# Performance work log

Measured on AMD Instinct MI355X. Metric: run time of the kernel, lower is better.

The kernel has to match this reference:

```python
import jax, jax.numpy as jnp
import numpy as np

D_MODEL = 1024
NUM_HEADS = 16
HEAD_DIM = D_MODEL // NUM_HEADS
THETA = 10000.0


def _trunc_normal(key, shape, std):
    # approximate trunc_normal_(a=-3std, b=3std) by clipping
    return jnp.clip(jax.random.normal(key, shape) * std, -3 * std, 3 * std)


def setup_inputs() -> dict:
    key = jax.random.key(0)
    ks = jax.random.split(key, 6)
    B, S = 2, 2048
    x = jax.random.normal(ks[0], (B, S, D_MODEL), dtype=jnp.float32)
    token_positions = jnp.sort(
        jax.random.randint(ks[1], (B, S), 0, 2048), axis=-1
    ).astype(jnp.int64)
    std = float(np.sqrt(2.0 / (D_MODEL + D_MODEL)))
    Wq = _trunc_normal(ks[2], (D_MODEL, D_MODEL), std)
    Wk = _trunc_normal(ks[3], (D_MODEL, D_MODEL), std)
    Wv = _trunc_normal(ks[4], (D_MODEL, D_MODEL), std)
    Wo = _trunc_normal(ks[5], (D_MODEL, D_MODEL), std)
    return {"x": x, "Wq": Wq, "Wk": Wk, "Wv": Wv, "Wo": Wo,
            "token_positions": token_positions}


def _rope(x, positions):
    # x: (b, h, s, d), positions: (b, s)
    d = x.shape[-1]
    inv_freq = THETA ** (-jnp.arange(0, d, 2, dtype=jnp.float32) / d)  # (d/2,)
    angles = positions.astype(jnp.float32)[:, None, :, None] * inv_freq  # (b,1,s,d/2)
    cos, sin = jnp.cos(angles), jnp.sin(angles)
    x_even, x_odd = x[..., 0::2], x[..., 1::2]
    out_even = x_even * cos - x_odd * sin
    out_odd = x_even * sin + x_odd * cos
    # interleave back: (..., d/2, 2) -> (..., d)
    return jnp.stack([out_even, out_odd], axis=-1).reshape(x.shape)


def reference(x, Wq, Wk, Wv, Wo, token_positions):
    B, S, _ = x.shape
    H, Dh = NUM_HEADS, HEAD_DIM
    # projections: einsum '... i, o i -> ... o'
    q = jnp.einsum('bsi,oi->bso', x, Wq).reshape(B, S, H, Dh).transpose(0, 2, 1, 3)
    k = jnp.einsum('bsi,oi->bso', x, Wk).reshape(B, S, H, Dh).transpose(0, 2, 1, 3)
    v = jnp.einsum('bsi,oi->bso', x, Wv).reshape(B, S, H, Dh).transpose(0, 2, 1, 3)
    q = _rope(q, token_positions)
    k = _rope(k, token_positions)
    scores = jnp.einsum('bhqd,bhkd->bhqk', q.astype(jnp.float32),
                        k.astype(jnp.float32)) / jnp.sqrt(
        jnp.asarray(Dh, dtype=jnp.float32))
    causal = jnp.tril(jnp.ones((S, S), dtype=bool))
    scores = jnp.where(causal, scores, -jnp.inf)
    attn = jax.nn.softmax(scores, axis=-1)
    out = jnp.einsum('bhqk,bhkd->bhqd', attn, v.astype(jnp.float32)).astype(x.dtype)
    out = out.transpose(0, 2, 1, 3).reshape(B, S, H * Dh)
    return jnp.einsum('bsi,oi->bso', out, Wo)
```

## Files before the change

kernel.cpp:

```cpp
#include <hip/hip_runtime.h>
#include <hip/hip_bf16.h>

#define DMODEL 1024
#define NHEADS 16
#define HDIM   64
#define BATCH  2
#define SEQ    2048
#define XELEMS ((size_t)BATCH * SEQ * DMODEL)
#define WELEMS ((size_t)DMODEL * DMODEL)

typedef __attribute__((ext_vector_type(8))) __bf16 bf16x8;
typedef __attribute__((ext_vector_type(4))) float  f32x4;
typedef __attribute__((ext_vector_type(2))) float  f32x2;
typedef __attribute__((ext_vector_type(4))) unsigned int   u32x4;
typedef __attribute__((ext_vector_type(4))) unsigned short u16x4;
typedef __attribute__((ext_vector_type(8))) unsigned short u16x8;

typedef const __attribute__((address_space(1))) void* gas_t;
typedef __attribute__((address_space(3))) void* las_t;

static __device__ __forceinline__ unsigned short f2bf(float f) {
  return __builtin_bit_cast(unsigned short, __float2bfloat16(f));
}
static __device__ __forceinline__ float bf2f(unsigned short u) {
  return __bfloat162float(__builtin_bit_cast(__hip_bfloat16, u));
}

__global__ __launch_bounds__(64) void probe_kernel(const unsigned int* __restrict__ x,
                                                   const int* __restrict__ pos,
                                                   int* __restrict__ flags) {
  const int lane = threadIdx.x;
  int bad = 0;
#pragma unroll
  for (int i = 0; i < 32; ++i) {
    const unsigned int u = x[lane * 32 + i];
    if (((u >> 23) & 0xFFu) == 0xFFu) bad++;
  }
  int zodd = 0;
#pragma unroll
  for (int i = 0; i < 4; ++i)
    if (pos[lane * 8 + 2 * i + 1] == 0) zodd++;
#pragma unroll
  for (int s = 1; s < 64; s <<= 1) {
    bad  += __shfl_xor(bad, s);
    zodd += __shfl_xor(zodd, s);
  }
  if (lane == 0) {
    flags[0] = (bad < 64) ? 1 : 0;
    flags[1] = (zodd >= 200) ? 1 : 0;
  }
}

__global__ __launch_bounds__(256) void rope_table_kernel(const int* __restrict__ pos,
                                                         const int* __restrict__ flags,
                                                         float* __restrict__ tab) {
  const int i = blockIdx.x * 256 + threadIdx.x;
  const int pd = i & 31, rs = i >> 5;
  const int pv = flags[1] ? pos[2 * rs] : pos[rs];
  const float ang = (float)pv * exp2f(-(float)pd * 0.41524101186092026f);
  f32x2 t; t[0] = cosf(ang); t[1] = sinf(ang);
  *(f32x2*)&tab[2 * i] = t;
}

__global__ __launch_bounds__(256) void conv_kernel(
    const void* __restrict__ x,
    const void* __restrict__ w0, const void* __restrict__ w1,
    const void* __restrict__ w2, const void* __restrict__ w3,
    unsigned short* __restrict__ dst, const int* __restrict__ flags) {
  const size_t e = ((size_t)blockIdx.x * 256 + threadIdx.x) * 8;
  const void* src;
  size_t off;
  if (e < XELEMS) { src = x; off = e; }
  else {
    const size_t r = e - XELEMS;
    const int wi = (int)(r >> 20);
    src = (wi == 0) ? w0 : (wi == 1) ? w1 : (wi == 2) ? w2 : w3;
    off = r & (WELEMS - 1);
  }
  if (flags[0]) {
    const float* s = (const float*)src + off;
    const f32x4 a = *(const f32x4*)(s);
    const f32x4 b = *(const f32x4*)(s + 4);
    u16x8 o8;
#pragma unroll
    for (int j = 0; j < 4; ++j) o8[j] = f2bf(a[j]);
#pragma unroll
    for (int j = 0; j < 4; ++j) o8[4 + j] = f2bf(b[j]);
    *(u16x8*)(dst + e) = o8;
  } else {
    *(u32x4*)(dst + e) = *(const u32x4*)((const unsigned short*)src + off);
  }
}

__device__ __forceinline__ void gemm_core(const unsigned short* __restrict__ Ag,
                                          const unsigned short* __restrict__ Bg,
                                          unsigned short* As, unsigned short* Bs,
                                          int bm, int bn, f32x4 acc[4][4]) {
  const int tid = threadIdx.x;
  const int lane = tid & 63;
  const int w  = tid >> 6;
  const int wm = w >> 1, wn = w & 1;
  const int c = lane & 15, g = lane >> 4;
  const int r0 = tid >> 2;
  const int s0 = (tid & 3) * 8;

  auto stage = [&](int buf, int k0) {
    unsigned short* ad = As + buf * 4096;
    unsigned short* bd = Bs + buf * 4096;
    __builtin_amdgcn_global_load_lds((gas_t)(Ag + (size_t)(bm + r0) * DMODEL + k0 + s0),
                                     (las_t)(ad + tid * 8), 16, 0, 0);
    __builtin_amdgcn_global_load_lds((gas_t)(Ag + (size_t)(bm + r0 + 64) * DMODEL + k0 + s0),
                                     (las_t)(ad + (tid + 256) * 8), 16, 0, 0);
    __builtin_amdgcn_global_load_lds((gas_t)(Bg + (size_t)(bn + r0) * DMODEL + k0 + s0),
                                     (las_t)(bd + tid * 8), 16, 0, 0);
    __builtin_amdgcn_global_load_lds((gas_t)(Bg + (size_t)(bn + r0 + 64) * DMODEL + k0 + s0),
                                     (las_t)(bd + (tid + 256) * 8), 16, 0, 0);
  };

  stage(0, 0);
  __syncthreads();
  for (int k0 = 0; k0 < DMODEL; k0 += 32) {
    const int cur = (k0 >> 5) & 1;
    if (k0 + 32 < DMODEL) stage(cur ^ 1, k0 + 32);
    const unsigned short* ar = As + cur * 4096;
    const unsigned short* br = Bs + cur * 4096;
    bf16x8 af[4], bfr[4];
#pragma unroll
    for (int m = 0; m < 4; ++m)
      af[m] = *(const bf16x8*)&ar[(wm * 64 + m * 16 + c) * 32 + g * 8];
#pragma unroll
    for (int n = 0; n < 4; ++n)
      bfr[n] = *(const bf16x8*)&br[(wn * 64 + n * 16 + c) * 32 + g * 8];
    __builtin_amdgcn_s_setprio(1);
#pragma unroll
    for (int m = 0; m < 4; ++m)
#pragma unroll
      for (int n = 0; n < 4; ++n)
        acc[m][n] = __builtin_amdgcn_mfma_f32_16x16x32_bf16(af[m], bfr[n], acc[m][n], 0, 0, 0);
    __builtin_amdgcn_s_setprio(0);
    __syncthreads();
  }
}

__global__ __launch_bounds__(256) void qkv_gemm_kernel(
    const unsigned short* __restrict__ x,
    const unsigned short* __restrict__ Wq, const unsigned short* __restrict__ Wk,
    const unsigned short* __restrict__ Wv,
    unsigned short* __restrict__ qo, unsigned short* __restrict__ ko,
    unsigned short* __restrict__ vto) {
  __shared__ unsigned short As[2 * 128 * 32];
  __shared__ unsigned short Bs[2 * 128 * 32];
  const int z = blockIdx.z;
  const unsigned short* W = (z == 0) ? Wq : (z == 1) ? Wk : Wv;
  const int bm = blockIdx.x * 128, bn = blockIdx.y * 128;
  f32x4 acc[4][4];
#pragma unroll
  for (int m = 0; m < 4; ++m)
#pragma unroll
    for (int n = 0; n < 4; ++n)
#pragma unroll
      for (int j = 0; j < 4; ++j) acc[m][n][j] = 0.f;

  gemm_core(x, W, As, Bs, bm, bn, acc);

  const int tid = threadIdx.x, lane = tid & 63, w = tid >> 6;
  const int wm = w >> 1, wn = w & 1, c = lane & 15, g4 = lane >> 4;
#pragma unroll
  for (int m = 0; m < 4; ++m) {
#pragma unroll
    for (int n = 0; n < 4; ++n) {
      const int col = bn + wn * 64 + n * 16 + c;
      const int h = col >> 6, d = col & 63;
      const int row0 = bm + wm * 64 + m * 16 + g4 * 4;
      if (z == 2) {
        const int b = row0 >> 11, s0 = row0 & (SEQ - 1);
        u16x4 pk;
#pragma unroll
        for (int j = 0; j < 4; ++j) pk[j] = f2bf(acc[m][n][j]);
        *(u16x4*)&vto[((size_t)(b * NHEADS + h) * HDIM + d) * SEQ + s0] = pk;
      } else {
        unsigned short* dst = z ? ko : qo;
#pragma unroll
        for (int j = 0; j < 4; ++j) {
          const int row = row0 + j;
          const int b = row >> 11, s = row & (SEQ - 1);
          dst[((size_t)(b * NHEADS + h) * SEQ + s) * HDIM + d] = f2bf(acc[m][n][j]);
        }
      }
    }
  }
}

__global__ __launch_bounds__(256) void out_gemm_kernel(
    const unsigned short* __restrict__ A, const unsigned short* __restrict__ Wo,
    void* __restrict__ outv, const int* __restrict__ flags) {
  __shared__ unsigned short As[2 * 64 * 32];
  __shared__ unsigned short Bs[2 * 128 * 32];
  const int bm = blockIdx.x * 64, bn = blockIdx.y * 128;
  const int tid = threadIdx.x, lane = tid & 63, w = tid >> 6;
  const int c = lane & 15, g = lane >> 4;
  const int r0 = tid >> 2, s0 = (tid & 3) * 8;
  f32x4 acc[4][2];
#pragma unroll
  for (int m = 0; m < 4; ++m)
#pragma unroll
    for (int n = 0; n < 2; ++n)
#pragma unroll
      for (int j = 0; j < 4; ++j) acc[m][n][j] = 0.f;

  auto stage = [&](int buf, int k0) {
    __builtin_amdgcn_global_load_lds((gas_t)(A + (size_t)(bm + r0) * DMODEL + k0 + s0),
                                     (las_t)(As + buf * 2048 + tid * 8), 16, 0, 0);
    __builtin_amdgcn_global_load_lds((gas_t)(Wo + (size_t)(bn + r0) * DMODEL + k0 + s0),
                                     (las_t)(Bs + buf * 4096 + tid * 8), 16, 0, 0);
    __builtin_amdgcn_global_load_lds((gas_t)(Wo + (size_t)(bn + r0 + 64) * DMODEL + k0 + s0),
                                     (las_t)(Bs + buf * 4096 + (tid + 256) * 8), 16, 0, 0);
  };

  stage(0, 0);
  __syncthreads();
  for (int k0 = 0; k0 < DMODEL; k0 += 32) {
    const int cur = (k0 >> 5) & 1;
    if (k0 + 32 < DMODEL) stage(cur ^ 1, k0 + 32);
    const unsigned short* ar = As + cur * 2048;
    const unsigned short* br = Bs + cur * 4096;
    bf16x8 af[4], bfr[2];
#pragma unroll
    for (int m = 0; m < 4; ++m)
      af[m] = *(const bf16x8*)&ar[(m * 16 + c) * 32 + g * 8];
#pragma unroll
    for (int n = 0; n < 2; ++n)
      bfr[n] = *(const bf16x8*)&br[(w * 32 + n * 16 + c) * 32 + g * 8];
    __builtin_amdgcn_s_setprio(1);
#pragma unroll
    for (int m = 0; m < 4; ++m)
#pragma unroll
      for (int n = 0; n < 2; ++n)
        acc[m][n] = __builtin_amdgcn_mfma_f32_16x16x32_bf16(af[m], bfr[n], acc[m][n], 0, 0, 0);
    __builtin_amdgcn_s_setprio(0);
    __syncthreads();
  }

  const int f32o = flags[0];
  if (f32o) {
    float* out = (float*)outv;
#pragma unroll
    for (int m = 0; m < 4; ++m)
#pragma unroll
      for (int n = 0; n < 2; ++n) {
        const int col = bn + w * 32 + n * 16 + c;
#pragma unroll
        for (int j = 0; j < 4; ++j) {
          const int row = bm + m * 16 + g * 4 + j;
          out[(size_t)row * DMODEL + col] = acc[m][n][j];
        }
      }
  } else {
    unsigned short* out = (unsigned short*)outv;
#pragma unroll
    for (int m = 0; m < 4; ++m)
#pragma unroll
      for (int n = 0; n < 2; ++n) {
        const int col = bn + w * 32 + n * 16 + c;
#pragma unroll
        for (int j = 0; j < 4; ++j) {
          const int row = bm + m * 16 + g * 4 + j;
          out[(size_t)row * DMODEL + col] = f2bf(acc[m][n][j]);
        }
      }
  }
}

__global__ __launch_bounds__(256) void rope_kernel(unsigned short* __restrict__ q,
                                                   unsigned short* __restrict__ k,
                                                   const float* __restrict__ tab) {
  const int idx = blockIdx.x * 256 + threadIdx.x;
  const int tsel = idx >> 21;
  const int p = idx & ((1 << 21) - 1);
  const int j = p & 31;
  const int s = (p >> 5) & (SEQ - 1);
  const int bh = p >> 16;
  const int b = bh >> 4;
  unsigned short* base = tsel ? k : q;
  const float sc = tsel ? 1.0f : 0.125f;
  const f32x2 t = *(const f32x2*)&tab[(((size_t)(b * SEQ + s)) * 32 + j) * 2];
  const float cs = t[0], sn = t[1];
  unsigned int* wp = (unsigned int*)base + ((p >> 5) * 32 + j);
  const unsigned int u = *wp;
  const float e = bf2f((unsigned short)(u & 0xffffu));
  const float o = bf2f((unsigned short)(u >> 16));
  *wp = (unsigned int)f2bf((e * cs - o * sn) * sc) |
        ((unsigned int)f2bf((e * sn + o * cs) * sc) << 16);
}

#define MNEG -1e30f
#define QBLK 64
#define LOG2E 1.4426950408889634f

template<int BUF>
__device__ __forceinline__ void flash_tile(
    int kt, int nkv, int qt, int qbase, int wq, int c, int g, int tid,
    const unsigned short* (&kp)[2], const unsigned short* (&vp)[2],
    unsigned short (&Ks)[2][64 * 64], unsigned short (&Vs)[2][64 * 64],
    unsigned short (&Ps)[64 * 64],
    const bf16x8 (&qf)[2], f32x4 (&acco)[4], float& m_r, float& l_r) {
  const int kvb = kt * 64;
  if (kt + 1 < nkv) {
#pragma unroll
    for (int i = 0; i < 2; ++i) {
      const int t8 = (tid + i * 256) * 8;
      __builtin_amdgcn_global_load_lds((gas_t)kp[i], (las_t)(Ks[BUF ^ 1] + t8), 16, 0, 0);
      __builtin_amdgcn_global_load_lds((gas_t)vp[i], (las_t)(Vs[BUF ^ 1] + t8), 16, 0, 0);
      kp[i] += 64 * HDIM;
      vp[i] += 64;
    }
  }

  f32x4 accs[4];
#pragma unroll
  for (int n = 0; n < 4; ++n)
#pragma unroll
    for (int j = 0; j < 4; ++j) accs[n][j] = 0.f;
  __builtin_amdgcn_s_setprio(1);
#pragma unroll
  for (int kk = 0; kk < 2; ++kk)
#pragma unroll
    for (int n = 0; n < 4; ++n) {
      const int r = n * 16 + c;
      const int sl = (kk * 4 + g) ^ (r & 7);
      const bf16x8 ak = *(const bf16x8*)&Ks[BUF][r * 64 + sl * 8];
      accs[n] = __builtin_amdgcn_mfma_f32_16x16x32_bf16(ak, qf[kk], accs[n], 0, 0, 0);
    }
  __builtin_amdgcn_s_setprio(0);

  const int qg = qbase + wq + c;
  if (kt == qt) {
#pragma unroll
    for (int n = 0; n < 4; ++n)
#pragma unroll
      for (int jj = 0; jj < 4; ++jj)
        if (kvb + n * 16 + g * 4 + jj > qg) accs[n][jj] = MNEG;
  }

  float rm = accs[0][0];
#pragma unroll
  for (int n = 0; n < 4; ++n)
#pragma unroll
    for (int jj = 0; jj < 4; ++jj) rm = fmaxf(rm, accs[n][jj]);
  rm = fmaxf(rm, __shfl_xor(rm, 16));
  rm = fmaxf(rm, __shfl_xor(rm, 32));
  if (!__all(rm <= m_r + 8.f)) {
    const float mn = fmaxf(m_r, rm);
    const float al = exp2f((m_r - mn) * LOG2E);
    l_r *= al;
#pragma unroll
    for (int n = 0; n < 4; ++n)
#pragma unroll
      for (int jj = 0; jj < 4; ++jj) acco[n][jj] *= al;
    m_r = mn;
  }
  float rs = 0.f;
#pragma unroll
  for (int n = 0; n < 4; ++n)
#pragma unroll
    for (int jj = 0; jj < 4; ++jj) {
      const float pv = exp2f((accs[n][jj] - m_r) * LOG2E);
      accs[n][jj] = pv;
      rs += pv;
    }
  rs += __shfl_xor(rs, 16);
  rs += __shfl_xor(rs, 32);
  l_r += rs;

  const int pr = wq + c;
  const int px = (pr & 7) << 3;
#pragma unroll
  for (int n = 0; n < 4; ++n) {
    u16x4 pk4;
#pragma unroll
    for (int jj = 0; jj < 4; ++jj) pk4[jj] = f2bf(accs[n][jj]);
    *(u16x4*)&Ps[pr * 64 + ((n * 16 + g * 4) ^ px)] = pk4;
  }

  __builtin_amdgcn_s_setprio(1);
#pragma unroll
  for (int kk = 0; kk < 2; ++kk) {
    const bf16x8 pb = *(const bf16x8*)&Ps[pr * 64 + ((kk * 32 + g * 8) ^ px)];
#pragma unroll
    for (int n = 0; n < 4; ++n) {
      const int r = n * 16 + c;
      const int sl = (kk * 4 + g) ^ (r & 7);
      const bf16x8 av = *(const bf16x8*)&Vs[BUF][r * 64 + sl * 8];
      acco[n] = __builtin_amdgcn_mfma_f32_16x16x32_bf16(av, pb, acco[n], 0, 0, 0);
    }
  }
  __builtin_amdgcn_s_setprio(0);
  __syncthreads();
}

__global__ __launch_bounds__(256, 4) void flash_kernel(
    const unsigned short* __restrict__ q, const unsigned short* __restrict__ k,
    const unsigned short* __restrict__ vt, unsigned short* __restrict__ o) {
  __shared__ unsigned short Ks[2][64 * 64];
  __shared__ unsigned short Vs[2][64 * 64];
  __shared__ unsigned short Ps[64 * 64];

  const int wg = blockIdx.x;
  const int qt = (SEQ / QBLK - 1) - (wg >> 5);
  const int bh = wg & 31;
  const int qbase = qt * QBLK;
  const int tid = threadIdx.x, lane = tid & 63, w = tid >> 6;
  const int c = lane & 15, g = lane >> 4;
  const int wq = w * 16;
  const size_t tb = (size_t)bh * SEQ * HDIM;

  bf16x8 qf[2];
#pragma unroll
  for (int kk = 0; kk < 2; ++kk)
    qf[kk] = *(const bf16x8*)(q + tb + (size_t)(qbase + wq + c) * HDIM + kk * 32 + g * 8);

  const unsigned short* kp[2];
  const unsigned short* vp[2];
#pragma unroll
  for (int i = 0; i < 2; ++i) {
    const int t = tid + i * 256;
    const int r = t >> 3;
    const int sl = (t & 7) ^ (r & 7);
    kp[i] = k + tb + (size_t)r * HDIM + sl * 8;
    vp[i] = vt + tb + (size_t)r * SEQ + sl * 8;
  }
#pragma unroll
  for (int i = 0; i < 2; ++i) {
    const int t8 = (tid + i * 256) * 8;
    __builtin_amdgcn_global_load_lds((gas_t)kp[i], (las_t)(Ks[0] + t8), 16, 0, 0);
    __builtin_amdgcn_global_load_lds((gas_t)vp[i], (las_t)(Vs[0] + t8), 16, 0, 0);
    kp[i] += 64 * HDIM;
    vp[i] += 64;
  }
  __syncthreads();

  f32x4 acco[4];
#pragma unroll
  for (int n = 0; n < 4; ++n)
#pragma unroll
    for (int j = 0; j < 4; ++j) acco[n][j] = 0.f;
  float m_r = MNEG, l_r = 0.f;

  const int nkv = qt + 1;
  int kt = 0;
  for (; kt + 2 <= nkv; kt += 2) {
    flash_tile<0>(kt,     nkv, qt, qbase, wq, c, g, tid, kp, vp, Ks, Vs, Ps, qf, acco, m_r, l_r);
    flash_tile<1>(kt + 1, nkv, qt, qbase, wq, c, g, tid, kp, vp, Ks, Vs, Ps, qf, acco, m_r, l_r);
  }
  if (kt < nkv)
    flash_tile<0>(kt, nkv, qt, qbase, wq, c, g, tid, kp, vp, Ks, Vs, Ps, qf, acco, m_r, l_r);

  const float rl = 1.f / fmaxf(l_r, 1e-20f);
  const int b = bh >> 4, h = bh & 15;
  const int srow = qbase + wq + c;
#pragma unroll
  for (int n = 0; n < 4; ++n) {
    u16x4 pk;
#pragma unroll
    for (int jj = 0; jj < 4; ++jj) pk[jj] = f2bf(acco[n][jj] * rl);
    *(u16x4*)&o[(size_t)(b * SEQ + srow) * DMODEL + h * 64 + n * 16 + g * 4] = pk;
  }
}

extern "C" void kernel_launch(void* const* d_in, const int* in_sizes, int n_in,
                              void* d_out, int out_size, void* d_ws, size_t ws_size,
                              hipStream_t stream) {
  (void)in_sizes; (void)n_in; (void)out_size; (void)ws_size;
  const size_t MB = (size_t)1 << 20;
  char* ws = (char*)d_ws;
  unsigned short* xb  = (unsigned short*)(ws);
  unsigned short* Wqb = (unsigned short*)(ws + 8 * MB);
  unsigned short* Wkb = (unsigned short*)(ws + 10 * MB);
  unsigned short* Wvb = (unsigned short*)(ws + 12 * MB);
  unsigned short* Wob = (unsigned short*)(ws + 14 * MB);
  unsigned short* qw  = (unsigned short*)(ws + 16 * MB);
  unsigned short* kw  = (unsigned short*)(ws + 24 * MB);
  unsigned short* vtw = (unsigned short*)(ws + 32 * MB);
  int* flags          = (int*)(ws + 40 * MB);
  float* tab          = (float*)(ws + 40 * MB + 4096);
  unsigned short* ow  = xb;

  const dim3 blk(256);
  probe_kernel<<<1, 64, 0, stream>>>((const unsigned int*)d_in[0], (const int*)d_in[5], flags);
  rope_table_kernel<<<512, blk, 0, stream>>>((const int*)d_in[5], flags, tab);
  conv_kernel<<<4096, blk, 0, stream>>>(d_in[0], d_in[1], d_in[2], d_in[3], d_in[4], xb, flags);
  qkv_gemm_kernel<<<dim3(32, 8, 3), blk, 0, stream>>>(xb, Wqb, Wkb, Wvb, qw, kw, vtw);
  rope_kernel<<<16384, blk, 0, stream>>>(qw, kw, tab);
  flash_kernel<<<dim3(1024), blk, 0, stream>>>(qw, kw, vtw, ow);
  out_gemm_kernel<<<dim3(64, 8), blk, 0, stream>>>(ow, Wob, d_out, flags);
}
```

Baseline: 123.7 us.

## Load K and V fragments directly from global into registers in flash kernel

Drops the double-buffered LDS staging of K and V tiles (global_load_lds plus a per-tile __syncthreads). Each wave now loads its MFMA operand fragments for K and V straight from global memory into registers every KV tile. This removes LDS traffic and block-wide barriers, but each of the four waves now fetches the same K/V data separately, which relies on L1/L2 hits. Loads are also no longer prefetched a tile ahead, so global latency may be exposed.

```diff
diff --git a/kernel.cpp b/kernel.cpp
--- a/kernel.cpp
+++ b/kernel.cpp
@@ -297,112 +297,9 @@
 #define QBLK 64
 #define LOG2E 1.4426950408889634f
 
-template<int BUF>
-__device__ __forceinline__ void flash_tile(
-    int kt, int nkv, int qt, int qbase, int wq, int c, int g, int tid,
-    const unsigned short* (&kp)[2], const unsigned short* (&vp)[2],
-    unsigned short (&Ks)[2][64 * 64], unsigned short (&Vs)[2][64 * 64],
-    unsigned short (&Ps)[64 * 64],
-    const bf16x8 (&qf)[2], f32x4 (&acco)[4], float& m_r, float& l_r) {
-  const int kvb = kt * 64;
-  if (kt + 1 < nkv) {
-#pragma unroll
-    for (int i = 0; i < 2; ++i) {
-      const int t8 = (tid + i * 256) * 8;
-      __builtin_amdgcn_global_load_lds((gas_t)kp[i], (las_t)(Ks[BUF ^ 1] + t8), 16, 0, 0);
-      __builtin_amdgcn_global_load_lds((gas_t)vp[i], (las_t)(Vs[BUF ^ 1] + t8), 16, 0, 0);
-      kp[i] += 64 * HDIM;
-      vp[i] += 64;
-    }
-  }
-
-  f32x4 accs[4];
-#pragma unroll
-  for (int n = 0; n < 4; ++n)
-#pragma unroll
-    for (int j = 0; j < 4; ++j) accs[n][j] = 0.f;
-  __builtin_amdgcn_s_setprio(1);
-#pragma unroll
-  for (int kk = 0; kk < 2; ++kk)
-#pragma unroll
-    for (int n = 0; n < 4; ++n) {
-      const int r = n * 16 + c;
-      const int sl = (kk * 4 + g) ^ (r & 7);
-      const bf16x8 ak = *(const bf16x8*)&Ks[BUF][r * 64 + sl * 8];
-      accs[n] = __builtin_amdgcn_mfma_f32_16x16x32_bf16(ak, qf[kk], accs[n], 0, 0, 0);
-    }
-  __builtin_amdgcn_s_setprio(0);
-
-  const int qg = qbase + wq + c;
-  if (kt == qt) {
-#pragma unroll
-    for (int n = 0; n < 4; ++n)
-#pragma unroll
-      for (int jj = 0; jj < 4; ++jj)
-        if (kvb + n * 16 + g * 4 + jj > qg) accs[n][jj] = MNEG;
-  }
-
-  float rm = accs[0][0];
-#pragma unroll
-  for (int n = 0; n < 4; ++n)
-#pragma unroll
-    for (int jj = 0; jj < 4; ++jj) rm = fmaxf(rm, accs[n][jj]);
-  rm = fmaxf(rm, __shfl_xor(rm, 16));
-  rm = fmaxf(rm, __shfl_xor(rm, 32));
-  if (!__all(rm <= m_r + 8.f)) {
-    const float mn = fmaxf(m_r, rm);
-    const float al = exp2f((m_r - mn) * LOG2E);
-    l_r *= al;
-#pragma unroll
-    for (int n = 0; n < 4; ++n)
-#pragma unroll
-      for (int jj = 0; jj < 4; ++jj) acco[n][jj] *= al;
-    m_r = mn;
-  }
-  float rs = 0.f;
-#pragma unroll
-  for (int n = 0; n < 4; ++n)
-#pragma unroll
-    for (int jj = 0; jj < 4; ++jj) {
-      const float pv = exp2f((accs[n][jj] - m_r) * LOG2E);
-      accs[n][jj] = pv;
-      rs += pv;
-    }
-  rs += __shfl_xor(rs, 16);
-  rs += __shfl_xor(rs, 32);
-  l_r += rs;
-
-  const int pr = wq + c;
-  const int px = (pr & 7) << 3;
-#pragma unroll
-  for (int n = 0; n < 4; ++n) {
-    u16x4 pk4;
-#pragma unroll
-    for (int jj = 0; jj < 4; ++jj) pk4[jj] = f2bf(accs[n][jj]);
-    *(u16x4*)&Ps[pr * 64 + ((n * 16 + g * 4) ^ px)] = pk4;
-  }
-
-  __builtin_amdgcn_s_setprio(1);
-#pragma unroll
-  for (int kk = 0; kk < 2; ++kk) {
-    const bf16x8 pb = *(const bf16x8*)&Ps[pr * 64 + ((kk * 32 + g * 8) ^ px)];
-#pragma unroll
-    for (int n = 0; n < 4; ++n) {
-      const int r = n * 16 + c;
-      const int sl = (kk * 4 + g) ^ (r & 7);
-      const bf16x8 av = *(const bf16x8*)&Vs[BUF][r * 64 + sl * 8];
-      acco[n] = __builtin_amdgcn_mfma_f32_16x16x32_bf16(av, pb, acco[n], 0, 0, 0);
-    }
-  }
-  __builtin_amdgcn_s_setprio(0);
-  __syncthreads();
-}
-
 __global__ __launch_bounds__(256, 4) void flash_kernel(
     const unsigned short* __restrict__ q, const unsigned short* __restrict__ k,
     const unsigned short* __restrict__ vt, unsigned short* __restrict__ o) {
-  __shared__ unsigned short Ks[2][64 * 64];
-  __shared__ unsigned short Vs[2][64 * 64];
   __shared__ unsigned short Ps[64 * 64];
 
   const int wg = blockIdx.x;
@@ -419,25 +316,8 @@
   for (int kk = 0; kk < 2; ++kk)
     qf[kk] = *(const bf16x8*)(q + tb + (size_t)(qbase + wq + c) * HDIM + kk * 32 + g * 8);
 
-  const unsigned short* kp[2];
-  const unsigned short* vp[2];
-#pragma unroll
-  for (int i = 0; i < 2; ++i) {
-    const int t = tid + i * 256;
-    const int r = t >> 3;
-    const int sl = (t & 7) ^ (r & 7);
-    kp[i] = k + tb + (size_t)r * HDIM + sl * 8;
-    vp[i] = vt + tb + (size_t)r * SEQ + sl * 8;
-  }
-#pragma unroll
-  for (int i = 0; i < 2; ++i) {
-    const int t8 = (tid + i * 256) * 8;
-    __builtin_amdgcn_global_load_lds((gas_t)kp[i], (las_t)(Ks[0] + t8), 16, 0, 0);
-    __builtin_amdgcn_global_load_lds((gas_t)vp[i], (las_t)(Vs[0] + t8), 16, 0, 0);
-    kp[i] += 64 * HDIM;
-    vp[i] += 64;
-  }
-  __syncthreads();
+  const unsigned short* kbase = k + tb + (size_t)(c)*HDIM + g * 8;
+  const unsigned short* vbase = vt + tb + (size_t)(c)*SEQ + g * 8;
 
   f32x4 acco[4];
 #pragma unroll
@@ -446,14 +326,97 @@
     for (int j = 0; j < 4; ++j) acco[n][j] = 0.f;
   float m_r = MNEG, l_r = 0.f;
 
+  const int pr = wq + c;
+  const int px = (pr & 7) << 3;
+
   const int nkv = qt + 1;
-  int kt = 0;
-  for (; kt + 2 <= nkv; kt += 2) {
-    flash_tile<0>(kt,     nkv, qt, qbase, wq, c, g, tid, kp, vp, Ks, Vs, Ps, qf, acco, m_r, l_r);
-    flash_tile<1>(kt + 1, nkv, qt, qbase, wq, c, g, tid, kp, vp, Ks, Vs, Ps, qf, acco, m_r, l_r);
-  }
-  if (kt < nkv)
-    flash_tile<0>(kt, nkv, qt, qbase, wq, c, g, tid, kp, vp, Ks, Vs, Ps, qf, acco, m_r, l_r);
+  for (int kt = 0; kt < nkv; ++kt) {
+    const int kvb = kt * 64;
+
+    bf16x8 ak[2][4];
+#pragma unroll
+    for (int kk = 0; kk < 2; ++kk)
+#pragma unroll
+      for (int n = 0; n < 4; ++n)
+        ak[kk][n] = *(const bf16x8*)(kbase + (size_t)(kvb + n * 16) * HDIM + kk * 32);
+
+    f32x4 accs[4];
+#pragma unroll
+    for (int n = 0; n < 4; ++n)
+#pragma unroll
+      for (int j = 0; j < 4; ++j) accs[n][j] = 0.f;
+    __builtin_amdgcn_s_setprio(1);
+#pragma unroll
+    for (int kk = 0; kk < 2; ++kk)
+#pragma unroll
+      for (int n = 0; n < 4; ++n)
+        accs[n] = __builtin_amdgcn_mfma_f32_16x16x32_bf16(ak[kk][n], qf[kk], accs[n], 0, 0, 0);
+    __builtin_amdgcn_s_setprio(0);
+
+    bf16x8 av[2][4];
+#pragma unroll
+    for (int kk = 0; kk < 2; ++kk)
+#pragma unroll
+      for (int n = 0; n < 4; ++n)
+        av[kk][n] = *(const bf16x8*)(vbase + (size_t)(n * 16) * SEQ + kvb + kk * 32);
+
+    const int qg = qbase + wq + c;
+    if (kt == qt) {
+#pragma unroll
+      for (int n = 0; n < 4; ++n)
+#pragma unroll
+        for (int jj = 0; jj < 4; ++jj)
+          if (kvb + n * 16 + g * 4 + jj > qg) accs[n][jj] = MNEG;
+    }
+
+    float rm = accs[0][0];
+#pragma unroll
+    for (int n = 0; n < 4; ++n)
+#pragma unroll
+      for (int jj = 0; jj < 4; ++jj) rm = fmaxf(rm, accs[n][jj]);
+    rm = fmaxf(rm, __shfl_xor(rm, 16));
+    rm = fmaxf(rm, __shfl_xor(rm, 32));
+    if (!__all(rm <= m_r + 8.f)) {
+      const float mn = fmaxf(m_r, rm);
+      const float al = exp2f((m_r - mn) * LOG2E);
+      l_r *= al;
+#pragma unroll
+      for (int n = 0; n < 4; ++n)
+#pragma unroll
+        for (int jj = 0; jj < 4; ++jj) acco[n][jj] *= al;
+      m_r = mn;
+    }
+    float rs = 0.f;
+#pragma unroll
+    for (int n = 0; n < 4; ++n)
+#pragma unroll
+      for (int jj = 0; jj < 4; ++jj) {
+        const float pv = exp2f((accs[n][jj] - m_r) * LOG2E);
+        accs[n][jj] = pv;
+        rs += pv;
+      }
+    rs += __shfl_xor(rs, 16);
+    rs += __shfl_xor(rs, 32);
+    l_r += rs;
+
+#pragma unroll
+    for (int n = 0; n < 4; ++n) {
+      u16x4 pk4;
+#pragma unroll
+      for (int jj = 0; jj < 4; ++jj) pk4[jj] = f2bf(accs[n][jj]);
+      *(u16x4*)&Ps[pr * 64 + ((n * 16 + g * 4) ^ px)] = pk4;
+    }
+
+    __builtin_amdgcn_s_setprio(1);
+#pragma unroll
+    for (int kk = 0; kk < 2; ++kk) {
+      const bf16x8 pb = *(const bf16x8*)&Ps[pr * 64 + ((kk * 32 + g * 8) ^ px)];
+#pragma unroll
+      for (int n = 0; n < 4; ++n)
+        acco[n] = __builtin_amdgcn_mfma_f32_16x16x32_bf16(av[kk][n], pb, acco[n], 0, 0, 0);
+    }
+    __builtin_amdgcn_s_setprio(0);
+  }
 
   const float rl = 1.f / fmaxf(l_r, 1e-20f);
   const int b = bh >> 4, h = bh & 15;
```

Result: slower. 221.6 us (+79.2%).

## Double flash attention query tile to 128 rows per workgroup

Applied to the files above, without the earlier changes.

Each workgroup now handles 128 query rows (each wave 32 rows as two 16-row MFMA tiles) rather than 64. K and V fragments are loaded from LDS once into registers and reused for both query sub-tiles, halving K/V global and LDS traffic per query row. The grid halves to 512 blocks and the launch-bounds occupancy hint drops to 2, which raises register pressure and reduces parallelism and load balance across the causal triangle.

```diff
diff --git a/kernel.cpp b/kernel.cpp
--- a/kernel.cpp
+++ b/kernel.cpp
@@ -294,16 +294,16 @@
 }
 
 #define MNEG -1e30f
-#define QBLK 64
 #define LOG2E 1.4426950408889634f
 
 template<int BUF>
 __device__ __forceinline__ void flash_tile(
-    int kt, int nkv, int qt, int qbase, int wq, int c, int g, int tid,
+    int kt, int nkv, int qt, int qbase, int wq32, int c, int g, int tid,
     const unsigned short* (&kp)[2], const unsigned short* (&vp)[2],
     unsigned short (&Ks)[2][64 * 64], unsigned short (&Vs)[2][64 * 64],
-    unsigned short (&Ps)[64 * 64],
-    const bf16x8 (&qf)[2], f32x4 (&acco)[4], float& m_r, float& l_r) {
+    unsigned short (&Ps)[128 * 64],
+    const bf16x8 (&qf)[2][2], f32x4 (&acco)[2][4],
+    float (&m_r)[2], float (&l_r)[2]) {
   const int kvb = kt * 64;
   if (kt + 1 < nkv) {
 #pragma unroll
@@ -316,108 +316,137 @@
     }
   }
 
-  f32x4 accs[4];
-#pragma unroll
-  for (int n = 0; n < 4; ++n)
-#pragma unroll
-    for (int j = 0; j < 4; ++j) accs[n][j] = 0.f;
-  __builtin_amdgcn_s_setprio(1);
+  bf16x8 ak[2][4];
 #pragma unroll
   for (int kk = 0; kk < 2; ++kk)
 #pragma unroll
     for (int n = 0; n < 4; ++n) {
       const int r = n * 16 + c;
       const int sl = (kk * 4 + g) ^ (r & 7);
-      const bf16x8 ak = *(const bf16x8*)&Ks[BUF][r * 64 + sl * 8];
-      accs[n] = __builtin_amdgcn_mfma_f32_16x16x32_bf16(ak, qf[kk], accs[n], 0, 0, 0);
-    }
+      ak[kk][n] = *(const bf16x8*)&Ks[BUF][r * 64 + sl * 8];
+    }
+
+  f32x4 accs[2][4];
+#pragma unroll
+  for (int m = 0; m < 2; ++m)
+#pragma unroll
+    for (int n = 0; n < 4; ++n)
+#pragma unroll
+      for (int j = 0; j < 4; ++j) accs[m][n][j] = 0.f;
+  __builtin_amdgcn_s_setprio(1);
+#pragma unroll
+  for (int kk = 0; kk < 2; ++kk)
+#pragma unroll
+    for (int n = 0; n < 4; ++n)
+#pragma unroll
+      for (int m = 0; m < 2; ++m)
+        accs[m][n] = __builtin_amdgcn_mfma_f32_16x16x32_bf16(ak[kk][n], qf[m][kk], accs[m][n], 0, 0, 0);
   __builtin_amdgcn_s_setprio(0);
 
-  const int qg = qbase + wq + c;
-  if (kt == qt) {
-#pragma unroll
-    for (int n = 0; n < 4; ++n)
-#pragma unroll
-      for (int jj = 0; jj < 4; ++jj)
-        if (kvb + n * 16 + g * 4 + jj > qg) accs[n][jj] = MNEG;
-  }
-
-  float rm = accs[0][0];
-#pragma unroll
-  for (int n = 0; n < 4; ++n)
-#pragma unroll
-    for (int jj = 0; jj < 4; ++jj) rm = fmaxf(rm, accs[n][jj]);
-  rm = fmaxf(rm, __shfl_xor(rm, 16));
-  rm = fmaxf(rm, __shfl_xor(rm, 32));
-  if (!__all(rm <= m_r + 8.f)) {
-    const float mn = fmaxf(m_r, rm);
-    const float al = exp2f((m_r - mn) * LOG2E);
-    l_r *= al;
-#pragma unroll
-    for (int n = 0; n < 4; ++n)
-#pragma unroll
-      for (int jj = 0; jj < 4; ++jj) acco[n][jj] *= al;
-    m_r = mn;
-  }
-  float rs = 0.f;
-#pragma unroll
-  for (int n = 0; n < 4; ++n)
-#pragma unroll
-    for (int jj = 0; jj < 4; ++jj) {
-      const float pv = exp2f((accs[n][jj] - m_r) * LOG2E);
-      accs[n][jj] = pv;
-      rs += pv;
-    }
-  rs += __shfl_xor(rs, 16);
-  rs += __shfl_xor(rs, 32);
-  l_r += rs;
-
-  const int pr = wq + c;
-  const int px = (pr & 7) << 3;
-#pragma unroll
-  for (int n = 0; n < 4; ++n) {
-    u16x4 pk4;
-#pragma unroll
-    for (int jj = 0; jj < 4; ++jj) pk4[jj] = f2bf(accs[n][jj]);
-    *(u16x4*)&Ps[pr * 64 + ((n * 16 + g * 4) ^ px)] = pk4;
-  }
-
-  __builtin_amdgcn_s_setprio(1);
-#pragma unroll
-  for (int kk = 0; kk < 2; ++kk) {
-    const bf16x8 pb = *(const bf16x8*)&Ps[pr * 64 + ((kk * 32 + g * 8) ^ px)];
+  bf16x8 av[2][4];
+#pragma unroll
+  for (int kk = 0; kk < 2; ++kk)
 #pragma unroll
     for (int n = 0; n < 4; ++n) {
       const int r = n * 16 + c;
       const int sl = (kk * 4 + g) ^ (r & 7);
-      const bf16x8 av = *(const bf16x8*)&Vs[BUF][r * 64 + sl * 8];
-      acco[n] = __builtin_amdgcn_mfma_f32_16x16x32_bf16(av, pb, acco[n], 0, 0, 0);
-    }
-  }
+      av[kk][n] = *(const bf16x8*)&Vs[BUF][r * 64 + sl * 8];
+    }
+
+  if (kt >= 2 * qt) {
+#pragma unroll
+    for (int m = 0; m < 2; ++m) {
+      const int qg = qbase + wq32 + m * 16 + c;
+#pragma unroll
+      for (int n = 0; n < 4; ++n)
+#pragma unroll
+        for (int jj = 0; jj < 4; ++jj)
+          if (kvb + n * 16 + g * 4 + jj > qg) accs[m][n][jj] = MNEG;
+    }
+  }
+
+#pragma unroll
+  for (int m = 0; m < 2; ++m) {
+    float rm = accs[m][0][0];
+#pragma unroll
+    for (int n = 0; n < 4; ++n)
+#pragma unroll
+      for (int jj = 0; jj < 4; ++jj) rm = fmaxf(rm, accs[m][n][jj]);
+    rm = fmaxf(rm, __shfl_xor(rm, 16));
+    rm = fmaxf(rm, __shfl_xor(rm, 32));
+    if (!__all(rm <= m_r[m] + 8.f)) {
+      const float mn = fmaxf(m_r[m], rm);
+      const float al = exp2f((m_r[m] - mn) * LOG2E);
+      l_r[m] *= al;
+#pragma unroll
+      for (int n = 0; n < 4; ++n)
+#pragma unroll
+        for (int jj = 0; jj < 4; ++jj) acco[m][n][jj] *= al;
+      m_r[m] = mn;
+    }
+    float rs = 0.f;
+#pragma unroll
+    for (int n = 0; n < 4; ++n)
+#pragma unroll
+      for (int jj = 0; jj < 4; ++jj) {
+        const float pv = exp2f((accs[m][n][jj] - m_r[m]) * LOG2E);
+        accs[m][n][jj] = pv;
+        rs += pv;
+      }
+    rs += __shfl_xor(rs, 16);
+    rs += __shfl_xor(rs, 32);
+    l_r[m] += rs;
+
+    const int pr = wq32 + m * 16 + c;
+    const int px = (pr & 7) << 3;
+#pragma unroll
+    for (int n = 0; n < 4; ++n) {
+      u16x4 pk4;
+#pragma unroll
+      for (int jj = 0; jj < 4; ++jj) pk4[jj] = f2bf(accs[m][n][jj]);
+      *(u16x4*)&Ps[pr * 64 + ((n * 16 + g * 4) ^ px)] = pk4;
+    }
+  }
+
+  __builtin_amdgcn_s_setprio(1);
+#pragma unroll
+  for (int kk = 0; kk < 2; ++kk)
+#pragma unroll
+    for (int m = 0; m < 2; ++m) {
+      const int pr = wq32 + m * 16 + c;
+      const int px = (pr & 7) << 3;
+      const bf16x8 pb = *(const bf16x8*)&Ps[pr * 64 + ((kk * 32 + g * 8) ^ px)];
+#pragma unroll
+      for (int n = 0; n < 4; ++n)
+        acco[m][n] = __builtin_amdgcn_mfma_f32_16x16x32_bf16(av[kk][n], pb, acco[m][n], 0, 0, 0);
+    }
   __builtin_amdgcn_s_setprio(0);
   __syncthreads();
 }
 
-__global__ __launch_bounds__(256, 4) void flash_kernel(
+__global__ __launch_bounds__(256, 2) void flash_kernel(
     const unsigned short* __restrict__ q, const unsigned short* __restrict__ k,
     const unsigned short* __restrict__ vt, unsigned short* __restrict__ o) {
   __shared__ unsigned short Ks[2][64 * 64];
   __shared__ unsigned short Vs[2][64 * 64];
-  __shared__ unsigned short Ps[64 * 64];
+  __shared__ unsigned short Ps[128 * 64];
 
   const int wg = blockIdx.x;
-  const int qt = (SEQ / QBLK - 1) - (wg >> 5);
+  const int qt = (SEQ / 128 - 1) - (wg >> 5);
   const int bh = wg & 31;
-  const int qbase = qt * QBLK;
+  const int qbase = qt * 128;
   const int tid = threadIdx.x, lane = tid & 63, w = tid >> 6;
   const int c = lane & 15, g = lane >> 4;
-  const int wq = w * 16;
+  const int wq32 = w * 32;
   const size_t tb = (size_t)bh * SEQ * HDIM;
 
-  bf16x8 qf[2];
-#pragma unroll
-  for (int kk = 0; kk < 2; ++kk)
-    qf[kk] = *(const bf16x8*)(q + tb + (size_t)(qbase + wq + c) * HDIM + kk * 32 + g * 8);
+  bf16x8 qf[2][2];
+#pragma unroll
+  for (int m = 0; m < 2; ++m)
+#pragma unroll
+    for (int kk = 0; kk < 2; ++kk)
+      qf[m][kk] = *(const bf16x8*)(q + tb + (size_t)(qbase + wq32 + m * 16 + c) * HDIM +
+                                   kk * 32 + g * 8);
 
   const unsigned short* kp[2];
   const unsigned short* vp[2];
@@ -439,31 +468,33 @@
   }
   __syncthreads();
 
-  f32x4 acco[4];
-#pragma unroll
-  for (int n = 0; n < 4; ++n)
-#pragma unroll
-    for (int j = 0; j < 4; ++j) acco[n][j] = 0.f;
-  float m_r = MNEG, l_r = 0.f;
-
-  const int nkv = qt + 1;
-  int kt = 0;
-  for (; kt + 2 <= nkv; kt += 2) {
-    flash_tile<0>(kt,     nkv, qt, qbase, wq, c, g, tid, kp, vp, Ks, Vs, Ps, qf, acco, m_r, l_r);
-    flash_tile<1>(kt + 1, nkv, qt, qbase, wq, c, g, tid, kp, vp, Ks, Vs, Ps, qf, acco, m_r, l_r);
-  }
-  if (kt < nkv)
-    flash_tile<0>(kt, nkv, qt, qbase, wq, c, g, tid, kp, vp, Ks, Vs, Ps, qf, acco, m_r, l_r);
-
-  const float rl = 1.f / fmaxf(l_r, 1e-20f);
+  f32x4 acco[2][4];
+#pragma unroll
+  for (int m = 0; m < 2; ++m)
+#pragma unroll
+    for (int n = 0; n < 4; ++n)
+#pragma unroll
+      for (int j = 0; j < 4; ++j) acco[m][n][j] = 0.f;
+  float m_r[2] = {MNEG, MNEG}, l_r[2] = {0.f, 0.f};
+
+  const int nkv = 2 * qt + 2;
+  for (int kt = 0; kt < nkv; kt += 2) {
+    flash_tile<0>(kt,     nkv, qt, qbase, wq32, c, g, tid, kp, vp, Ks, Vs, Ps, qf, acco, m_r, l_r);
+    flash_tile<1>(kt + 1, nkv, qt, qbase, wq32, c, g, tid, kp, vp, Ks, Vs, Ps, qf, acco, m_r, l_r);
+  }
+
   const int b = bh >> 4, h = bh & 15;
-  const int srow = qbase + wq + c;
-#pragma unroll
-  for (int n = 0; n < 4; ++n) {
-    u16x4 pk;
-#pragma unroll
-    for (int jj = 0; jj < 4; ++jj) pk[jj] = f2bf(acco[n][jj] * rl);
-    *(u16x4*)&o[(size_t)(b * SEQ + srow) * DMODEL + h * 64 + n * 16 + g * 4] = pk;
+#pragma unroll
+  for (int m = 0; m < 2; ++m) {
+    const float rl = 1.f / fmaxf(l_r[m], 1e-20f);
+    const int srow = qbase + wq32 + m * 16 + c;
+#pragma unroll
+    for (int n = 0; n < 4; ++n) {
+      u16x4 pk;
+#pragma unroll
+      for (int jj = 0; jj < 4; ++jj) pk[jj] = f2bf(acco[m][n][jj] * rl);
+      *(u16x4*)&o[(size_t)(b * SEQ + srow) * DMODEL + h * 64 + n * 16 + g * 4] = pk;
+    }
   }
 }
 
@@ -491,6 +522,6 @@
   conv_kernel<<<4096, blk, 0, stream>>>(d_in[0], d_in[1], d_in[2], d_in[3], d_in[4], xb, flags);
   qkv_gemm_kernel<<<dim3(32, 8, 3), blk, 0, stream>>>(xb, Wqb, Wkb, Wvb, qw, kw, vtw);
   rope_kernel<<<16384, blk, 0, stream>>>(qw, kw, tab);
-  flash_kernel<<<dim3(1024), blk, 0, stream>>>(qw, kw, vtw, ow);
+  flash_kernel<<<dim3(512), blk, 0, stream>>>(qw, kw, vtw, ow);
   out_gemm_kernel<<<dim3(64, 8), blk, 0, stream>>>(ow, Wob, d_out, flags);
 }
```

New measurement: 136.9 us. +10.6%, slower.
